# Kernel optimization log

Hardware: AMD Instinct MI355X
Metric: run time of the kernel (lower is better)

Reference implementation:

```python
import jax, jax.numpy as jnp
import numpy as np

N_NODES = 100000
IN_DIM = 256
HIDDEN = 512
N_INC = 1000000   # incidence (gather/scatter) list length
N_SEG = 100000    # number of hyperedges / segments


def setup_inputs() -> dict:
    key = jax.random.key(0)
    ks = jax.random.split(key, 6)
    x = jax.random.normal(ks[0], (N_NODES, IN_DIM), dtype=jnp.float32)
    target_nodes = jax.random.randint(ks[1], (N_INC,), 0, N_NODES, dtype=jnp.int32)
    target_ids = jnp.sort(jax.random.randint(ks[2], (N_INC,), 0, N_SEG, dtype=jnp.int32))
    # Linear params (PyTorch stores [out,in]; we keep [in,out] and matmul directly)
    W1 = jax.random.normal(ks[3], (IN_DIM, HIDDEN), dtype=jnp.float32) * (1.0 / np.sqrt(IN_DIM))
    b1 = jnp.zeros((HIDDEN,), dtype=jnp.float32)
    W2 = jax.random.normal(ks[4], (HIDDEN, 1), dtype=jnp.float32) * (1.0 / np.sqrt(HIDDEN))
    b2 = jnp.zeros((1,), dtype=jnp.float32)
    return {"x": x, "target_nodes": target_nodes, "target_ids": target_ids,
            "num_segments": N_SEG, "W1": W1, "b1": b1, "W2": W2, "b2": b2}


def reference(x, target_nodes, target_ids, num_segments, W1, b1, W2, b2):
    # gather node features, scatter-sum into segments (hyperedges)
    gathered = x[target_nodes, :]                                   # [N_INC, IN_DIM]
    Z = jax.ops.segment_sum(gathered, target_ids,
                            num_segments=num_segments)              # [N_SEG, IN_DIM]
    Z = jnp.maximum(Z @ W1 + b1, 0.0)                               # linear + relu
    # dropout is identity in eval mode
    Z = Z @ W2 + b2                                                 # [N_SEG, 1]
    return jax.nn.sigmoid(Z)[:, 0]                                  # squeeze(-1)
```

## Files before the change

kernel.cpp:

```cpp
#include <hip/hip_runtime.h>
#include <hip/hip_bf16.h>
#include <math.h>

#define N_NODES   100000
#define IN_DIM    256
#define HIDDEN    512
#define N_INC     1000000
#define N_SEG     100000

typedef __attribute__((ext_vector_type(8))) short bf16x8;
typedef __attribute__((ext_vector_type(4))) float f32x4;

__device__ __forceinline__ unsigned short f2bf(float f) {
  unsigned int u = __builtin_bit_cast(unsigned int, f);
  u += 0x7FFFu + ((u >> 16) & 1u);
  return (unsigned short)(u >> 16);
}
__device__ __forceinline__ float bflo(unsigned int u) {
  return __builtin_bit_cast(float, u << 16);
}
__device__ __forceinline__ float bfhi(unsigned int u) {
  return __builtin_bit_cast(float, u & 0xFFFF0000u);
}
__device__ __forceinline__ unsigned pack2(float a, float b) {
  return (unsigned)f2bf(a) | ((unsigned)f2bf(b) << 16);
}

__device__ __forceinline__ void gload_lds16(const void* g, void* l) {
  __builtin_amdgcn_global_load_lds(
      (const __attribute__((address_space(1))) unsigned int*)g,
      (__attribute__((address_space(3))) unsigned int*)l, 16, 0, 0);
}

#define XBF_BLOCKS    25000
#define STARTS_BLOCKS 391
#define W1T_BLOCKS    128

__global__ void k_prep(const float* __restrict__ x, unsigned short* __restrict__ xb,
                       const int* __restrict__ ids, int* __restrict__ starts,
                       const float* __restrict__ W1, unsigned short* __restrict__ W1t) {
  const int b = blockIdx.x;
  const int tid = threadIdx.x;
  if (b < XBF_BLOCKS) {
    size_t idx = (size_t)b * 256 + tid;
    float4 v = *(const float4*)(x + idx * 4);
    uint2 p;
    p.x = pack2(v.x, v.y);
    p.y = pack2(v.z, v.w);
    *(uint2*)(xb + idx * 4) = p;
  } else if (b < XBF_BLOCKS + STARTS_BLOCKS) {
    int s = (b - XBF_BLOCKS) * 256 + tid;
    if (s > N_SEG) return;
    int lo = 0, hi = N_INC;
    while (lo < hi) {
      int mid = (lo + hi) >> 1;
      if (ids[mid] < s) lo = mid + 1; else hi = mid;
    }
    starts[s] = lo;
  } else {
    int idx = (b - XBF_BLOCKS - STARTS_BLOCKS) * 256 + tid;
    int k  = idx >> 7;
    int c4 = idx & 127;
    float4 v = *(const float4*)(W1 + (size_t)k * HIDDEN + c4 * 4);
    W1t[(c4 * 4 + 0) * IN_DIM + k] = f2bf(v.x);
    W1t[(c4 * 4 + 1) * IN_DIM + k] = f2bf(v.y);
    W1t[(c4 * 4 + 2) * IN_DIM + k] = f2bf(v.z);
    W1t[(c4 * 4 + 3) * IN_DIM + k] = f2bf(v.w);
  }
}

#define ACC8(v)                                                        \
  acc0 += bflo((v).x); acc1 += bfhi((v).x);                            \
  acc2 += bflo((v).y); acc3 += bfhi((v).y);                            \
  acc4 += bflo((v).z); acc5 += bfhi((v).z);                            \
  acc6 += bflo((v).w); acc7 += bfhi((v).w);

__global__ void k_segsum(const unsigned short* __restrict__ xb, const int* __restrict__ nodes,
                         const int* __restrict__ starts, unsigned short* __restrict__ Zb) {
  int wave = threadIdx.x >> 6;
  int lane = threadIdx.x & 63;
  int s = blockIdx.x * 4 + wave;
  if (s >= N_SEG) return;
  const int beg = starts[s];
  const int end = starts[s + 1];
  const int half = lane >> 5;
  const int sl   = lane & 31;
  const unsigned short* base = xb + sl * 8;
  float acc0 = 0.f, acc1 = 0.f, acc2 = 0.f, acc3 = 0.f;
  float acc4 = 0.f, acc5 = 0.f, acc6 = 0.f, acc7 = 0.f;
  int j = beg + half;
  for (; j + 6 < end; j += 8) {
    int n0 = nodes[j], n1 = nodes[j + 2], n2 = nodes[j + 4], n3 = nodes[j + 6];
    uint4 v0 = *(const uint4*)(base + (size_t)n0 * IN_DIM);
    uint4 v1 = *(const uint4*)(base + (size_t)n1 * IN_DIM);
    uint4 v2 = *(const uint4*)(base + (size_t)n2 * IN_DIM);
    uint4 v3 = *(const uint4*)(base + (size_t)n3 * IN_DIM);
    ACC8(v0); ACC8(v1); ACC8(v2); ACC8(v3);
  }
  for (; j < end; j += 2) {
    int n0 = nodes[j];
    uint4 v0 = *(const uint4*)(base + (size_t)n0 * IN_DIM);
    ACC8(v0);
  }
  acc0 += __shfl_xor(acc0, 32, 64);
  acc1 += __shfl_xor(acc1, 32, 64);
  acc2 += __shfl_xor(acc2, 32, 64);
  acc3 += __shfl_xor(acc3, 32, 64);
  acc4 += __shfl_xor(acc4, 32, 64);
  acc5 += __shfl_xor(acc5, 32, 64);
  acc6 += __shfl_xor(acc6, 32, 64);
  acc7 += __shfl_xor(acc7, 32, 64);
  if (half == 0) {
    uint4 p;
    p.x = pack2(acc0, acc1);
    p.y = pack2(acc2, acc3);
    p.z = pack2(acc4, acc5);
    p.w = pack2(acc6, acc7);
    *(uint4*)(Zb + (size_t)s * IN_DIM + sl * 8) = p;
  }
}

__global__ __launch_bounds__(256, 3) void k_mlp(
    const unsigned short* __restrict__ Zb, const unsigned short* __restrict__ W1t,
    const float* __restrict__ b1, const float* __restrict__ W2,
    const float* __restrict__ b2, float* __restrict__ out) {
  __shared__ __align__(16) unsigned short Bf[8][4][64][8];
  const int tid  = threadIdx.x;
  const int wave = tid >> 6;
  const int lane = tid & 63;
  const int m0   = blockIdx.x * 128 + wave * 32;

  uint4 a[2][8];
  const int arow = m0 + (lane & 15);
  const int ak   = (lane >> 4) * 8;
  #pragma unroll
  for (int kc = 0; kc < 8; ++kc) {
    #pragma unroll
    for (int rf = 0; rf < 2; ++rf) {
      int row = arow + rf * 16;
      if (row < N_SEG)
        a[rf][kc] = *(const uint4*)(Zb + (size_t)row * IN_DIM + kc * 32 + ak);
      else
        a[rf][kc] = make_uint4(0u, 0u, 0u, 0u);
    }
  }

  const unsigned short* wsrc = W1t + (size_t)(wave * 16 + (lane & 15)) * IN_DIM
                                   + (lane >> 4) * 8;

  float logit[2][4];
  #pragma unroll
  for (int rf = 0; rf < 2; ++rf)
    #pragma unroll
    for (int e = 0; e < 4; ++e) logit[rf][e] = 0.f;

  for (int nt = 0; nt < 8; ++nt) {
    const int c0 = nt * 64;
    #pragma unroll
    for (int it = 0; it < 8; ++it)
      gload_lds16(wsrc + (size_t)c0 * IN_DIM + it * 32, &Bf[it][wave][lane][0]);
    __syncthreads();

    f32x4 acc[2][4];
    #pragma unroll
    for (int rf = 0; rf < 2; ++rf)
      #pragma unroll
      for (int cf = 0; cf < 4; ++cf) acc[rf][cf] = (f32x4){0.f, 0.f, 0.f, 0.f};

    #pragma unroll
    for (int kc = 0; kc < 8; ++kc) {
      #pragma unroll
      for (int cf = 0; cf < 4; ++cf) {
        bf16x8 bv = *(const bf16x8*)&Bf[kc][cf][lane][0];
        #pragma unroll
        for (int rf = 0; rf < 2; ++rf) {
          bf16x8 av = __builtin_bit_cast(bf16x8, a[rf][kc]);
          acc[rf][cf] = __builtin_amdgcn_mfma_f32_16x16x32_bf16(av, bv, acc[rf][cf], 0, 0, 0);
        }
      }
    }
    __syncthreads();

    #pragma unroll
    for (int cf = 0; cf < 4; ++cf) {
      int cc = c0 + cf * 16 + (lane & 15);
      float bb = b1[cc];
      float w2 = W2[cc];
      #pragma unroll
      for (int rf = 0; rf < 2; ++rf)
        #pragma unroll
        for (int e = 0; e < 4; ++e) {
          float h = acc[rf][cf][e] + bb;
          h = h > 0.f ? h : 0.f;
          logit[rf][e] = fmaf(h, w2, logit[rf][e]);
        }
    }
  }
  #pragma unroll
  for (int rf = 0; rf < 2; ++rf)
    #pragma unroll
    for (int e = 0; e < 4; ++e) {
      float v = logit[rf][e];
      v += __shfl_xor(v, 1, 64);
      v += __shfl_xor(v, 2, 64);
      v += __shfl_xor(v, 4, 64);
      v += __shfl_xor(v, 8, 64);
      logit[rf][e] = v;
    }
  if ((lane & 15) == 0) {
    float bb2 = b2[0];
    #pragma unroll
    for (int rf = 0; rf < 2; ++rf)
      #pragma unroll
      for (int e = 0; e < 4; ++e) {
        int row = m0 + rf * 16 + (lane >> 4) * 4 + e;
        if (row < N_SEG)
          out[row] = 1.f / (1.f + expf(-(logit[rf][e] + bb2)));
      }
  }
}

extern "C" void kernel_launch(void* const* d_in, const int* in_sizes, int n_in,
                              void* d_out, int out_size, void* d_ws, size_t ws_size,
                              hipStream_t stream) {
  const float* x   = (const float*)d_in[0];
  const int* nodes = (const int*)d_in[1];
  const int* ids   = (const int*)d_in[2];
  const float* W1  = (const float*)d_in[4];
  const float* b1  = (const float*)d_in[5];
  const float* W2  = (const float*)d_in[6];
  const float* b2  = (const float*)d_in[7];
  float* out       = (float*)d_out;

  char* ws = (char*)d_ws;
  int* starts = (int*)ws;
  size_t off = (((size_t)(N_SEG + 1) * sizeof(int)) + 1023) & ~(size_t)1023;
  unsigned short* Zb = (unsigned short*)(ws + off);
  off += (size_t)N_NODES * IN_DIM * sizeof(unsigned short);
  off = (off + 1023) & ~(size_t)1023;
  unsigned short* W1t = (unsigned short*)(ws + off);
  off += (size_t)HIDDEN * IN_DIM * sizeof(unsigned short);
  off = (off + 1023) & ~(size_t)1023;
  unsigned short* xb = (unsigned short*)(ws + off);

  k_prep<<<XBF_BLOCKS + STARTS_BLOCKS + W1T_BLOCKS, 256, 0, stream>>>(
      x, xb, ids, starts, W1, W1t);
  k_segsum<<<(N_SEG + 3) / 4, 256, 0, stream>>>(xb, nodes, starts, Zb);
  k_mlp<<<(N_SEG + 127) / 128, 256, 0, stream>>>(Zb, W1t, b1, W2, b2, out);
}
```

Baseline: 169.1 us.

## Double-buffer W1 tiles in MLP kernel with 512-thread blocks and packed bias/W2

New measurement: 149.5 us (median of 2 runs). 11.6% less time.

```diff
diff --git a/kernel.cpp b/kernel.cpp
--- a/kernel.cpp
+++ b/kernel.cpp
@@ -35,10 +35,13 @@
 #define XBF_BLOCKS    25000
 #define STARTS_BLOCKS 391
 #define W1T_BLOCKS    128
+#define BW2_BLOCKS    2
 
 __global__ void k_prep(const float* __restrict__ x, unsigned short* __restrict__ xb,
                        const int* __restrict__ ids, int* __restrict__ starts,
-                       const float* __restrict__ W1, unsigned short* __restrict__ W1t) {
+                       const float* __restrict__ W1, unsigned short* __restrict__ W1t,
+                       const float* __restrict__ b1, const float* __restrict__ W2,
+                       unsigned int* __restrict__ bw2) {
   const int b = blockIdx.x;
   const int tid = threadIdx.x;
   if (b < XBF_BLOCKS) {
@@ -57,7 +60,7 @@
       if (ids[mid] < s) lo = mid + 1; else hi = mid;
     }
     starts[s] = lo;
-  } else {
+  } else if (b < XBF_BLOCKS + STARTS_BLOCKS + W1T_BLOCKS) {
     int idx = (b - XBF_BLOCKS - STARTS_BLOCKS) * 256 + tid;
     int k  = idx >> 7;
     int c4 = idx & 127;
@@ -66,6 +69,9 @@
     W1t[(c4 * 4 + 1) * IN_DIM + k] = f2bf(v.y);
     W1t[(c4 * 4 + 2) * IN_DIM + k] = f2bf(v.z);
     W1t[(c4 * 4 + 3) * IN_DIM + k] = f2bf(v.w);
+  } else {
+    int c = (b - XBF_BLOCKS - STARTS_BLOCKS - W1T_BLOCKS) * 256 + tid;
+    if (c < HIDDEN) bw2[c] = pack2(b1[c], W2[c]);
   }
 }
 
@@ -120,15 +126,27 @@
   }
 }
 
-__global__ __launch_bounds__(256, 3) void k_mlp(
+__global__ __launch_bounds__(512, 3) void k_mlp(
     const unsigned short* __restrict__ Zb, const unsigned short* __restrict__ W1t,
-    const float* __restrict__ b1, const float* __restrict__ W2,
-    const float* __restrict__ b2, float* __restrict__ out) {
-  __shared__ __align__(16) unsigned short Bf[8][4][64][8];
+    const unsigned int* __restrict__ bw2, const float* __restrict__ b2,
+    float* __restrict__ out) {
+  __shared__ __align__(16) unsigned short Bf[2][8][4][64][8];
   const int tid  = threadIdx.x;
   const int wave = tid >> 6;
   const int lane = tid & 63;
-  const int m0   = blockIdx.x * 128 + wave * 32;
+  const int m0   = blockIdx.x * 256 + wave * 32;
+
+  const unsigned short* wsrc = W1t + (size_t)(lane & 15) * IN_DIM
+                                   + wave * 32 + (lane >> 4) * 8;
+
+  #pragma unroll
+  for (int j = 0; j < 4; ++j)
+    gload_lds16(wsrc + (size_t)(j * 16) * IN_DIM, &Bf[0][wave][j][lane][0]);
+
+  unsigned int bw2r[32];
+  #pragma unroll
+  for (int i = 0; i < 32; ++i)
+    bw2r[i] = bw2[(i >> 2) * 64 + (i & 3) * 16 + (lane & 15)];
 
   uint4 a[2][8];
   const int arow = m0 + (lane & 15);
@@ -145,21 +163,27 @@
     }
   }
 
-  const unsigned short* wsrc = W1t + (size_t)(wave * 16 + (lane & 15)) * IN_DIM
-                                   + (lane >> 4) * 8;
-
+  const float b2v = ((lane & 15) == 0) ? b2[0] : 0.f;
   float logit[2][4];
   #pragma unroll
   for (int rf = 0; rf < 2; ++rf)
     #pragma unroll
-    for (int e = 0; e < 4; ++e) logit[rf][e] = 0.f;
-
+    for (int e = 0; e < 4; ++e) logit[rf][e] = b2v;
+
+  #pragma unroll
   for (int nt = 0; nt < 8; ++nt) {
-    const int c0 = nt * 64;
-    #pragma unroll
-    for (int it = 0; it < 8; ++it)
-      gload_lds16(wsrc + (size_t)c0 * IN_DIM + it * 32, &Bf[it][wave][lane][0]);
-    __syncthreads();
+    const int cur = nt & 1;
+    if (nt < 7) {
+      const size_t csrc = (size_t)((nt + 1) * 64) * IN_DIM;
+      #pragma unroll
+      for (int j = 0; j < 4; ++j)
+        gload_lds16(wsrc + csrc + (size_t)(j * 16) * IN_DIM, &Bf[cur ^ 1][wave][j][lane][0]);
+      asm volatile("s_waitcnt vmcnt(4)" ::: "memory");
+    } else {
+      asm volatile("s_waitcnt vmcnt(0)" ::: "memory");
+    }
+    __builtin_amdgcn_s_barrier();
+    __builtin_amdgcn_sched_barrier(0);
 
     f32x4 acc[2][4];
     #pragma unroll
@@ -171,7 +195,7 @@
     for (int kc = 0; kc < 8; ++kc) {
       #pragma unroll
       for (int cf = 0; cf < 4; ++cf) {
-        bf16x8 bv = *(const bf16x8*)&Bf[kc][cf][lane][0];
+        bf16x8 bv = *(const bf16x8*)&Bf[cur][kc][cf][lane][0];
         #pragma unroll
         for (int rf = 0; rf < 2; ++rf) {
           bf16x8 av = __builtin_bit_cast(bf16x8, a[rf][kc]);
@@ -179,13 +203,12 @@
         }
       }
     }
-    __syncthreads();
 
     #pragma unroll
     for (int cf = 0; cf < 4; ++cf) {
-      int cc = c0 + cf * 16 + (lane & 15);
-      float bb = b1[cc];
-      float w2 = W2[cc];
+      unsigned int bw = bw2r[nt * 4 + cf];
+      float bb = bflo(bw);
+      float w2 = bfhi(bw);
       #pragma unroll
       for (int rf = 0; rf < 2; ++rf)
         #pragma unroll
@@ -195,7 +218,9 @@
           logit[rf][e] = fmaf(h, w2, logit[rf][e]);
         }
     }
-  }
+    __builtin_amdgcn_s_barrier();
+  }
+
   #pragma unroll
   for (int rf = 0; rf < 2; ++rf)
     #pragma unroll
@@ -208,14 +233,13 @@
       logit[rf][e] = v;
     }
   if ((lane & 15) == 0) {
-    float bb2 = b2[0];
     #pragma unroll
     for (int rf = 0; rf < 2; ++rf)
       #pragma unroll
       for (int e = 0; e < 4; ++e) {
         int row = m0 + rf * 16 + (lane >> 4) * 4 + e;
         if (row < N_SEG)
-          out[row] = 1.f / (1.f + expf(-(logit[rf][e] + bb2)));
+          out[row] = 1.f / (1.f + expf(-logit[rf][e]));
       }
   }
 }
@@ -241,10 +265,13 @@
   unsigned short* W1t = (unsigned short*)(ws + off);
   off += (size_t)HIDDEN * IN_DIM * sizeof(unsigned short);
   off = (off + 1023) & ~(size_t)1023;
+  unsigned int* bw2 = (unsigned int*)(ws + off);
+  off += (size_t)HIDDEN * sizeof(unsigned int);
+  off = (off + 1023) & ~(size_t)1023;
   unsigned short* xb = (unsigned short*)(ws + off);
 
-  k_prep<<<XBF_BLOCKS + STARTS_BLOCKS + W1T_BLOCKS, 256, 0, stream>>>(
-      x, xb, ids, starts, W1, W1t);
+  k_prep<<<XBF_BLOCKS + STARTS_BLOCKS + W1T_BLOCKS + BW2_BLOCKS, 256, 0, stream>>>(
+      x, xb, ids, starts, W1, W1t, b1, W2, bw2);
   k_segsum<<<(N_SEG + 3) / 4, 256, 0, stream>>>(xb, nodes, starts, Zb);
-  k_mlp<<<(N_SEG + 127) / 128, 256, 0, stream>>>(Zb, W1t, b1, W2, b2, out);
-}
+  k_mlp<<<(N_SEG + 255) / 256, 512, 0, stream>>>(Zb, W1t, bw2, b2, out);
+}
```
